# Kernel tuning notes

Hardware: AMD Instinct MI355X
Metric: run time of the kernel (lower is better)

The kernel has to match this reference:

```python
import jax, jax.numpy as jnp
import numpy as np

D_MODEL = 1024
N_HEADS = 16
D_K = D_MODEL // N_HEADS


def setup_inputs() -> dict:
    key = jax.random.key(0)
    ks = jax.random.split(key, 7)
    B, S = 2, 2048
    q = jax.random.normal(ks[0], (B, S, D_MODEL), dtype=jnp.float32)
    k = jax.random.normal(ks[1], (B, S, D_MODEL), dtype=jnp.float32)
    v = jax.random.normal(ks[2], (B, S, D_MODEL), dtype=jnp.float32)
    mask = jnp.ones((B, 1, S, S), dtype=bool)
    scale = 1.0 / np.sqrt(D_MODEL)
    w_q = jax.random.normal(ks[3], (D_MODEL, D_MODEL), dtype=jnp.float32) * scale
    w_k = jax.random.normal(ks[4], (D_MODEL, D_MODEL), dtype=jnp.float32) * scale
    w_v = jax.random.normal(ks[5], (D_MODEL, D_MODEL), dtype=jnp.float32) * scale
    w_o = jax.random.normal(ks[6], (D_MODEL, D_MODEL), dtype=jnp.float32) * scale
    return {"q": q, "k": k, "v": v, "mask": mask,
            "w_q": w_q, "w_k": w_k, "w_v": w_v, "w_o": w_o}


def reference(q, k, v, mask, w_q, w_k, w_v, w_o):
    B, S, _ = q.shape
    # projections (nn.Linear: x @ W^T, no bias)
    def split_heads(x):  # [B,S,D] -> [B,H,S,d_k]
        return x.reshape(B, -1, N_HEADS, D_K).transpose(0, 2, 1, 3)
    query = split_heads(q @ w_q.T)
    key_h = split_heads(k @ w_k.T)
    value = split_heads(v @ w_v.T)
    # naive scaled dot-product attention: full [B,H,S,S] scores materialized
    scores = jnp.einsum('bhqd,bhkd->bhqk', query, key_h) / jnp.sqrt(
        jnp.asarray(D_K, query.dtype))
    scores = jnp.where(mask, scores, jnp.asarray(-1e9, scores.dtype))
    attn = jax.nn.softmax(scores, axis=-1)  # dropout p=0.0 -> identity
    x = jnp.einsum('bhqk,bhkd->bhqd', attn, value)
    x = x.transpose(0, 2, 1, 3).reshape(B, S, N_HEADS * D_K)
    return x @ w_o.T
```

## Files before the change

### kernel.cpp

```cpp
#include <hip/hip_runtime.h>
#include <hip/hip_bf16.h>
#include <math.h>

typedef __bf16 bf16;
typedef __bf16 bf16x8 __attribute__((ext_vector_type(8)));
typedef float f32x4 __attribute__((ext_vector_type(4)));
typedef float f32x16 __attribute__((ext_vector_type(16)));
typedef unsigned u32x4 __attribute__((ext_vector_type(4)));

#define MFMA16(a, b, c) __builtin_amdgcn_mfma_f32_16x16x32_bf16((a), (b), (c), 0, 0, 0)
#define MFMA32(a, b, c) __builtin_amdgcn_mfma_f32_32x32x16_bf16((a), (b), (c), 0, 0, 0)

__device__ __forceinline__ void gl_lds16(const void* g, void* l) {
    __builtin_amdgcn_global_load_lds(
        (__attribute__((address_space(1))) void*)(g),
        (__attribute__((address_space(3))) void*)(l),
        16, 0, 0);
}

__device__ __forceinline__ unsigned cvt_pk_bf16(float lo, float hi) {
    unsigned r;
    asm("v_cvt_pk_bf16_f32 %0, %1, %2" : "=v"(r) : "v"(lo), "v"(hi));
    return r;
}

__global__ __launch_bounds__(256) void cvt7(
    const float* __restrict__ w0, const float* __restrict__ w1,
    const float* __restrict__ w2, const float* __restrict__ w3,
    const float* __restrict__ x0, const float* __restrict__ x1,
    const float* __restrict__ x2, bf16* __restrict__ dst) {
    const int z = blockIdx.y;
    const float* src;
    bf16* out;
    if (z < 4) {
        if (blockIdx.x >= 512) return;
        src = (z == 0) ? w0 : (z == 1) ? w1 : (z == 2) ? w2 : w3;
        out = dst + (size_t)z * 1048576;
    } else {
        src = (z == 4) ? x0 : (z == 5) ? x1 : x2;
        out = dst + 4 * 1048576 + (size_t)(z - 4) * 4194304;
    }
    const int i = (blockIdx.x * 256 + threadIdx.x) * 8;
    float4 a = ((const float4*)(src + i))[0];
    float4 b = ((const float4*)(src + i))[1];
    bf16x8 o;
    o[0] = (bf16)a.x; o[1] = (bf16)a.y; o[2] = (bf16)a.z; o[3] = (bf16)a.w;
    o[4] = (bf16)b.x; o[5] = (bf16)b.y; o[6] = (bf16)b.z; o[7] = (bf16)b.w;
    *(bf16x8*)(out + i) = o;
}

template <int EP>
__device__ __forceinline__ void gemm_bf(const bf16* __restrict__ A,
                                        const bf16* __restrict__ B,
                                        void* __restrict__ Cv,
                                        const int m0, const int n0,
                                        bf16* __restrict__ As,
                                        bf16* __restrict__ Bs) {
    constexpr int K = 1024;

    const int t = threadIdx.x;
    const int lane = t & 63;
    const int w = t >> 6;
    const int wm = (w >> 2) * 64;
    const int wn = (w & 3) * 32;
    const int lr = lane & 15;
    const int lq8 = (lane >> 4) * 8;
    const int rq = (lane >> 4) * 4;

    f32x4 acc[4][2] = {};

    const int srow = t >> 2;
    const int sch = (t & 3) * 8;
    char* lA = (char*)As;
    char* lB = (char*)Bs;

#define QSTAGE(buf, k0)                                                              \
    do {                                                                             \
        gl_lds16(A + (size_t)(m0 + srow) * K + (k0) + sch,                           \
                 lA + (buf) * 8192 + t * 16);                                        \
        gl_lds16(B + (size_t)(n0 + srow) * K + (k0) + sch,                           \
                 lB + (buf) * 8192 + t * 16);                                        \
    } while (0)

    QSTAGE(0, 0);
    __syncthreads();

    int cur = 0;
    for (int k0 = 0; k0 < K; k0 += 32) {
        if (k0 + 32 < K) QSTAGE(cur ^ 1, k0 + 32);

        bf16x8 af[4], bfr[2];
#pragma unroll
        for (int i = 0; i < 4; ++i)
            af[i]  = *(const bf16x8*)&As[cur * 4096 + (wm + i * 16 + lr) * 32 + lq8];
#pragma unroll
        for (int i = 0; i < 2; ++i)
            bfr[i] = *(const bf16x8*)&Bs[cur * 4096 + (wn + i * 16 + lr) * 32 + lq8];
#pragma unroll
        for (int mi = 0; mi < 4; ++mi)
#pragma unroll
            for (int ni = 0; ni < 2; ++ni)
                acc[mi][ni] = MFMA16(af[mi], bfr[ni], acc[mi][ni]);

        __syncthreads();
        cur ^= 1;
    }
#undef QSTAGE

#pragma unroll
    for (int mi = 0; mi < 4; ++mi) {
#pragma unroll
        for (int ni = 0; ni < 2; ++ni) {
#pragma unroll
            for (int r = 0; r < 4; ++r) {
                const int m = m0 + wm + mi * 16 + rq + r;
                const int n = n0 + wn + ni * 16 + lr;
                const float vv = acc[mi][ni][r];
                if constexpr (EP == 0) {
                    bf16* C = (bf16*)Cv;
                    const int b = m >> 11, s = m & 2047;
                    const int h = n >> 6,  d = n & 63;
                    C[(((size_t)(b * 16 + h)) * 2048 + s) * 64 + d] = (bf16)vv;
                } else if constexpr (EP == 1) {
                    float* C = (float*)Cv;
                    C[(size_t)m * 1024 + n] = vv;
                } else {
                    bf16* C = (bf16*)Cv;
                    C[((size_t)(n >> 11) * 1024 + m) * 2048 + (n & 2047)] = (bf16)vv;
                }
            }
        }
    }
}

__global__ __launch_bounds__(512, 6) void qkv_bf(
    const bf16* __restrict__ Xq, const bf16* __restrict__ Xk,
    const bf16* __restrict__ Xv, const bf16* __restrict__ Wc,
    bf16* __restrict__ Qb, bf16* __restrict__ Kb, bf16* __restrict__ Vb) {
    __shared__ __align__(16) bf16 As[2 * 128 * 32];
    __shared__ __align__(16) bf16 Bs[2 * 128 * 32];
    const int z = blockIdx.z;
    if (z == 0)
        gemm_bf<0>(Xq, Wc, Qb, blockIdx.x * 128, blockIdx.y * 128, As, Bs);
    else if (z == 1)
        gemm_bf<0>(Xk, Wc + 1048576, Kb, blockIdx.x * 128, blockIdx.y * 128, As, Bs);
    else
        gemm_bf<2>(Wc + 2 * 1048576, Xv, Vb, blockIdx.y * 128, blockIdx.x * 128, As, Bs);
}

__global__ __launch_bounds__(512, 4) void out_gemm(
    const bf16* __restrict__ X, const bf16* __restrict__ W, float* __restrict__ C) {
    constexpr int K = 1024;
    __shared__ __align__(16) bf16 As[2][128 * 32];
    __shared__ __align__(16) bf16 Bs[2][64 * 32];

    const int t = threadIdx.x;
    const int lane = t & 63;
    const int w = t >> 6;
    const int wm = (w >> 1) * 32;
    const int wn = (w & 1) * 32;
    const int lr = lane & 15;
    const int lq8 = (lane >> 4) * 8;
    const int rq = (lane >> 4) * 4;
    const int m0 = blockIdx.x * 128, n0 = blockIdx.y * 64;

    f32x4 acc[2][2] = {};

    const int srow = t >> 2;
    const int sch = (t & 3) * 8;
    char* lA = (char*)As;
    char* lB = (char*)Bs;

#define OSTAGE(buf, k0)                                                              \
    do {                                                                             \
        gl_lds16(X + (size_t)(m0 + srow) * K + (k0) + sch,                           \
                 lA + (buf) * 8192 + t * 16);                                        \
        if (t < 256)                                                                 \
            gl_lds16(W + (size_t)(n0 + srow) * K + (k0) + sch,                       \
                     lB + (buf) * 4096 + t * 16);                                    \
    } while (0)

    OSTAGE(0, 0);
    __syncthreads();

    int cur = 0;
    for (int k0 = 0; k0 < K; k0 += 32) {
        if (k0 + 32 < K) OSTAGE(cur ^ 1, k0 + 32);

        bf16x8 af[2], bfr[2];
#pragma unroll
        for (int i = 0; i < 2; ++i) {
            af[i]  = *(const bf16x8*)&As[cur][(wm + i * 16 + lr) * 32 + lq8];
            bfr[i] = *(const bf16x8*)&Bs[cur][(wn + i * 16 + lr) * 32 + lq8];
        }
#pragma unroll
        for (int mi = 0; mi < 2; ++mi)
#pragma unroll
            for (int ni = 0; ni < 2; ++ni)
                acc[mi][ni] = MFMA16(af[mi], bfr[ni], acc[mi][ni]);

        __syncthreads();
        cur ^= 1;
    }
#undef OSTAGE

#pragma unroll
    for (int mi = 0; mi < 2; ++mi)
#pragma unroll
        for (int ni = 0; ni < 2; ++ni)
#pragma unroll
            for (int r = 0; r < 4; ++r) {
                const int m = m0 + wm + mi * 16 + rq + r;
                const int n = n0 + wn + ni * 16 + lr;
                C[(size_t)m * 1024 + n] = acc[mi][ni][r];
            }
}

template <int MODE>
__device__ __forceinline__ void gemm_f32tok(const void* __restrict__ Av,
                                            const void* __restrict__ Bv,
                                            bf16* __restrict__ C,
                                            const int m0, const int n0,
                                            bf16* __restrict__ As,
                                            bf16* __restrict__ Bs) {
    constexpr int K = 1024;

    const int t = threadIdx.x;
    const int lane = t & 63;
    const int w = t >> 6;
    const int wm = (w & 1) * 64;
    const int wn = (w >> 1) * 64;
    const int lr = lane & 15;
    const int lq8 = (lane >> 4) * 8;
    const int rq = (lane >> 4) * 4;

    f32x4 acc[4][4] = {};
    const int srow = t >> 2;
    const int sch = (t & 3) * 8;
    const int ar = t >> 1;
    const int ac = (t & 1) * 16;
    char* lA = (char*)As;
    char* lB = (char*)Bs;

    for (int k0 = 0; k0 < K; k0 += 32) {
        if constexpr (MODE == 0) {
            const float* X = (const float*)Av;
            const float* p = X + (size_t)(m0 + ar) * K + k0 + ac;
            float4 f0 = ((const float4*)p)[0], f1 = ((const float4*)p)[1];
            float4 f2 = ((const float4*)p)[2], f3 = ((const float4*)p)[3];
            bf16x8 o0, o1;
            o0[0]=(bf16)f0.x; o0[1]=(bf16)f0.y; o0[2]=(bf16)f0.z; o0[3]=(bf16)f0.w;
            o0[4]=(bf16)f1.x; o0[5]=(bf16)f1.y; o0[6]=(bf16)f1.z; o0[7]=(bf16)f1.w;
            o1[0]=(bf16)f2.x; o1[1]=(bf16)f2.y; o1[2]=(bf16)f2.z; o1[3]=(bf16)f2.w;
            o1[4]=(bf16)f3.x; o1[5]=(bf16)f3.y; o1[6]=(bf16)f3.z; o1[7]=(bf16)f3.w;
            *(bf16x8*)&As[ar * 32 + ac]     = o0;
            *(bf16x8*)&As[ar * 32 + ac + 8] = o1;
        } else {
            const bf16* X = (const bf16*)Av;
            gl_lds16(X + (size_t)(m0 + srow) * K + k0 + sch,      lA + t * 16);
            gl_lds16(X + (size_t)(m0 + 64 + srow) * K + k0 + sch, lA + 4096 + t * 16);
        }
        if constexpr (MODE == 2) {
            const float* X = (const float*)Bv;
            const float* p = X + (size_t)(n0 + ar) * K + k0 + ac;
            float4 f0 = ((const float4*)p)[0], f1 = ((const float4*)p)[1];
            float4 f2 = ((const float4*)p)[2], f3 = ((const float4*)p)[3];
            bf16x8 o0, o1;
            o0[0]=(bf16)f0.x; o0[1]=(bf16)f0.y; o0[2]=(bf16)f0.z; o0[3]=(bf16)f0.w;
            o0[4]=(bf16)f1.x; o0[5]=(bf16)f1.y; o0[6]=(bf16)f1.z; o0[7]=(bf16)f1.w;
            o1[0]=(bf16)f2.x; o1[1]=(bf16)f2.y; o1[2]=(bf16)f2.z; o1[3]=(bf16)f2.w;
            o1[4]=(bf16)f3.x; o1[5]=(bf16)f3.y; o1[6]=(bf16)f3.z; o1[7]=(bf16)f3.w;
            *(bf16x8*)&Bs[ar * 32 + ac]     = o0;
            *(bf16x8*)&Bs[ar * 32 + ac + 8] = o1;
        } else {
            const bf16* W = (const bf16*)Bv;
            gl_lds16(W + (size_t)(n0 + srow) * K + k0 + sch,      lB + t * 16);
            gl_lds16(W + (size_t)(n0 + 64 + srow) * K + k0 + sch, lB + 4096 + t * 16);
        }
        __syncthreads();

        bf16x8 af[4], bfr[4];
#pragma unroll
        for (int i = 0; i < 4; ++i) {
            af[i]  = *(const bf16x8*)&As[(wm + i * 16 + lr) * 32 + lq8];
            bfr[i] = *(const bf16x8*)&Bs[(wn + i * 16 + lr) * 32 + lq8];
        }
#pragma unroll
        for (int mi = 0; mi < 4; ++mi)
#pragma unroll
            for (int ni = 0; ni < 4; ++ni)
                acc[mi][ni] = MFMA16(af[mi], bfr[ni], acc[mi][ni]);
        __syncthreads();
    }

#pragma unroll
    for (int mi = 0; mi < 4; ++mi) {
#pragma unroll
        for (int ni = 0; ni < 4; ++ni) {
#pragma unroll
            for (int r = 0; r < 4; ++r) {
                const int m = m0 + wm + mi * 16 + rq + r;
                const int n = n0 + wn + ni * 16 + lr;
                const float vv = acc[mi][ni][r];
                if constexpr (MODE == 0) {
                    const int b = m >> 11, s = m & 2047;
                    const int h = n >> 6,  d = n & 63;
                    C[(((size_t)(b * 16 + h)) * 2048 + s) * 64 + d] = (bf16)vv;
                } else {
                    C[((size_t)(n >> 11) * 1024 + m) * 2048 + (n & 2047)] = (bf16)vv;
                }
            }
        }
    }
}

__global__ __launch_bounds__(256, 2) void qkv_f32(
    const float* __restrict__ q, const float* __restrict__ k, const float* __restrict__ v,
    const bf16* __restrict__ Wc, bf16* __restrict__ Qb, bf16* __restrict__ Kb,
    bf16* __restrict__ Vb) {
    __shared__ __align__(16) bf16 As[128 * 32];
    __shared__ __align__(16) bf16 Bs[128 * 32];
    const int z = blockIdx.z;
    if (z == 0)
        gemm_f32tok<0>(q, Wc, Qb, blockIdx.x * 128, blockIdx.y * 128, As, Bs);
    else if (z == 1)
        gemm_f32tok<0>(k, Wc + 1048576, Kb, blockIdx.x * 128, blockIdx.y * 128, As, Bs);
    else
        gemm_f32tok<2>(Wc + 2 * 1048576, v, Vb, blockIdx.y * 128, blockIdx.x * 128, As, Bs);
}

__global__ __launch_bounds__(512, 4) void attn_kernel(
    const bf16* __restrict__ Qb, const bf16* __restrict__ Kb,
    const bf16* __restrict__ Vb, bf16* __restrict__ Xb) {
    constexpr int S = 2048;

    __shared__ __align__(16) bf16 smem[17408];

    const int t = threadIdx.x;
    const int lane = t & 63;
    const int w = t >> 6;
    const int wg = w & 3;
    const int kh = w >> 2;
    const int l31 = lane & 31;
    const int half = lane >> 5;

    const int lin = blockIdx.x;
    const int g = lin >> 3;
    const int bh = (lin & 7) + 8 * (g & 3);
    const int q0 = (g >> 2) * 128 + wg * 32;

    const bf16* Q  = Qb + (size_t)bh * S * 64;
    const bf16* Kh = Kb + (size_t)bh * S * 64;
    const bf16* Vh = Vb + (size_t)bh * 64 * S;

    const float qscale = 0.125f * 1.4426950408889634f;
    bf16x8 qf[4];
#pragma unroll
    for (int c = 0; c < 4; ++c) {
        bf16x8 v0 = *(const bf16x8*)(Q + (size_t)(q0 + l31) * 64 + c * 16 + half * 8);
#pragma unroll
        for (int e = 0; e < 8; ++e) v0[e] = (bf16)((float)v0[e] * qscale);
        qf[c] = v0;
    }

    f32x16 od[2] = {};
    float ls0 = 0.f, ls1 = 0.f, ls2 = 0.f, ls3 = 0.f;

    const int tt = t & 255;
    const int sr = tt >> 2;
    const int sc = (tt & 3) * 2;
    const bf16* pKg = Kh + ((size_t)kh * 1024 + sr) * 64 + sc * 8;
    const bf16* pVg = Vh + (size_t)sr * S + kh * 1024 + sc * 8;
    bf16* KsH = smem + kh * 4096;
    bf16* VsH = smem + 8192 + kh * 4096;
    int wKo[2];
#pragma unroll
    for (int c = 0; c < 2; ++c)
        wKo[c] = (sr >> 1) * 128 + ((((sr & 1) << 3) + sc + c) ^ ((sr >> 1) & 15)) * 8;

    bf16x8 pk[2], pv[2];
#pragma unroll
    for (int c = 0; c < 2; ++c) {
        pk[c] = *(const bf16x8*)(pKg + c * 8);
        pv[c] = *(const bf16x8*)(pVg + c * 8);
    }

    const int fbase = (l31 >> 1) * 128;
    const int fb8 = (l31 & 1) << 3;
    const int fsw = l31 >> 1;

    for (int j = 0; j < 16; ++j) {
        __syncthreads();
#pragma unroll
        for (int c = 0; c < 2; ++c) {
            *(bf16x8*)&KsH[wKo[c]] = pk[c];
            *(bf16x8*)&VsH[wKo[c]] = pv[c];
        }
        __syncthreads();

        f32x16 sacc[2] = {};
#pragma unroll
        for (int kt = 0; kt < 2; ++kt) {
#pragma unroll
            for (int c = 0; c < 4; ++c) {
                bf16x8 kf = *(const bf16x8*)
                    &KsH[kt * 2048 + fbase + ((fb8 + c * 2 + half) ^ fsw) * 8];
                sacc[kt] = MFMA32(kf, qf[c], sacc[kt]);
            }
        }

        if (j + 1 < 16) {
            pKg += 4096;
            pVg += 64;
#pragma unroll
            for (int c = 0; c < 2; ++c) {
                pk[c] = *(const bf16x8*)(pKg + c * 8);
                pv[c] = *(const bf16x8*)(pVg + c * 8);
            }
        }

#pragma unroll
        for (int kt = 0; kt < 2; ++kt) {
            float ex[16];
#pragma unroll
            for (int r = 0; r < 16; ++r)
                ex[r] = exp2f(sacc[kt][r]);
            ls0 += ex[0] + ex[4] + ex[8]  + ex[12];
            ls1 += ex[1] + ex[5] + ex[9]  + ex[13];
            ls2 += ex[2] + ex[6] + ex[10] + ex[14];
            ls3 += ex[3] + ex[7] + ex[11] + ex[15];

            unsigned pa[8];
#pragma unroll
            for (int c2 = 0; c2 < 2; ++c2) {
#pragma unroll
                for (int wd = 0; wd < 2; ++wd) {
                    unsigned x = cvt_pk_bf16(ex[c2 * 8 + wd * 2 + 0], ex[c2 * 8 + wd * 2 + 1]);
                    unsigned y = cvt_pk_bf16(ex[c2 * 8 + wd * 2 + 4], ex[c2 * 8 + wd * 2 + 5]);
                    asm("v_permlane32_swap_b32 %0, %1" : "+v"(x), "+v"(y));
                    pa[c2 * 4 + wd]     = x;
                    pa[c2 * 4 + wd + 2] = y;
                }
            }

#pragma unroll
            for (int c2 = 0; c2 < 2; ++c2) {
                u32x4 aw;
                aw[0] = pa[c2 * 4 + 0]; aw[1] = pa[c2 * 4 + 1];
                aw[2] = pa[c2 * 4 + 2]; aw[3] = pa[c2 * 4 + 3];
                bf16x8 ap = __builtin_bit_cast(bf16x8, aw);
#pragma unroll
                for (int dt = 0; dt < 2; ++dt) {
                    const int cgv = kt * 4 + c2 * 2 + half;
                    bf16x8 vf = *(const bf16x8*)
                        &VsH[dt * 2048 + fbase + ((fb8 + cgv) ^ fsw) * 8];
                    od[dt] = MFMA32(ap, vf, od[dt]);
                }
            }
        }
    }

    float lsum = ls0 + ls1 + ls2 + ls3;
    float ltot = lsum + __shfl_xor(lsum, 32);

    __syncthreads();
    float* fsm = (float*)smem;
    const int so = (wg * 64 + lane) * 34;
    if (kh == 1) {
        fsm[so + 32] = ltot;
#pragma unroll
        for (int r = 0; r < 16; ++r) {
            fsm[so + r]      = od[0][r];
            fsm[so + 16 + r] = od[1][r];
        }
    }
    __syncthreads();
    if (kh == 0) {
        ltot += fsm[so + 32];
        const float inv = 1.f / fmaxf(ltot, 1e-30f);
        const int b = bh >> 4, hh = bh & 15;
#pragma unroll
        for (int r = 0; r < 16; ++r) {
            const int qrow = (r & 3) + 8 * (r >> 2) + 4 * half;
            const float invr = __shfl(inv, qrow);
            const size_t base = ((size_t)(b * 2048 + q0 + qrow)) * 1024 + hh * 64;
            Xb[base + l31]      = (bf16)((od[0][r] + fsm[so + r]) * invr);
            Xb[base + 32 + l31] = (bf16)((od[1][r] + fsm[so + 16 + r]) * invr);
        }
    }
}

extern "C" void kernel_launch(void* const* d_in, const int* in_sizes, int n_in,
                              void* d_out, int out_size, void* d_ws, size_t ws_size,
                              hipStream_t stream) {
    const float* q  = (const float*)d_in[0];
    const float* k  = (const float*)d_in[1];
    const float* v  = (const float*)d_in[2];
    const float* wq = (const float*)d_in[4];
    const float* wk = (const float*)d_in[5];
    const float* wv = (const float*)d_in[6];
    const float* wo = (const float*)d_in[7];
    float* out = (float*)d_out;

    const bool big = ws_size >= (size_t)64 * 1024 * 1024;
    bf16* Wc = (bf16*)d_ws;
    const dim3 blk(256);

    if (big) {
        bf16* Xq = Wc + 4 * 1048576;
        bf16* Xk = Xq + 4194304;
        bf16* Xv = Xk + 4194304;
        bf16* Qb = Xv + 4194304;
        bf16* Kb = Qb + 4194304;
        bf16* Vb = Kb + 4194304;
        bf16* Xb = Vb + 4194304;
        cvt7<<<dim3(2048, 7), blk, 0, stream>>>(wq, wk, wv, wo, q, k, v, Wc);
        qkv_bf<<<dim3(32, 8, 3), dim3(512), 0, stream>>>(Xq, Xk, Xv, Wc, Qb, Kb, Vb);
        attn_kernel<<<dim3(512), dim3(512), 0, stream>>>(Qb, Kb, Vb, Xb);
        out_gemm<<<dim3(32, 16), dim3(512), 0, stream>>>(Xb, Wc + 3 * 1048576, out);
    } else {
        bf16* Qb = Wc + 4 * 1048576;
        bf16* Kb = Qb + 4194304;
        bf16* Vb = Kb + 4194304;
        bf16* Xb = Vb + 4194304;
        cvt7<<<dim3(512, 4), blk, 0, stream>>>(wq, wk, wv, wo, q, k, v, Wc);
        qkv_f32<<<dim3(32, 8, 3), blk, 0, stream>>>(q, k, v, Wc, Qb, Kb, Vb);
        attn_kernel<<<dim3(512), dim3(512), 0, stream>>>(Qb, Kb, Vb, Xb);
        out_gemm<<<dim3(32, 16), dim3(512), 0, stream>>>(Xb, Wc + 3 * 1048576, out);
    }
}
```

Before: 236.9 us.

## Fuse fp32-to-bf16 activation conversion into QKV projection GEMM staging

The QKV GEMM now reads the fp32 q/k/v activations directly. It loads them into registers during the prefetch stage and converts them to bf16 when writing LDS after the MFMA work. The separate conversion pass for activations is dropped, and cvt7 now converts only the weights. This removes a full write and read of three 4M-element bf16 activation buffers. In exchange, each fp32 tile is re-read once for every N-tile block, which doubles the global bytes on the activation side. Staging also goes through registers instead of direct global-to-LDS loads, which adds register pressure and VALU conversion work inside the main loop.

```diff
diff --git a/kernel.cpp b/kernel.cpp
--- a/kernel.cpp
+++ b/kernel.cpp
@@ -49,9 +49,9 @@
     *(bf16x8*)(out + i) = o;
 }
 
-template <int EP>
-__device__ __forceinline__ void gemm_bf(const bf16* __restrict__ A,
-                                        const bf16* __restrict__ B,
+template <int EP, int AF32, int BF32>
+__device__ __forceinline__ void gemm_bf(const void* __restrict__ Av,
+                                        const void* __restrict__ Bv,
                                         void* __restrict__ Cv,
                                         const int m0, const int n0,
                                         bf16* __restrict__ As,
@@ -74,20 +74,60 @@
     char* lA = (char*)As;
     char* lB = (char*)Bs;
 
-#define QSTAGE(buf, k0)                                                              \
-    do {                                                                             \
-        gl_lds16(A + (size_t)(m0 + srow) * K + (k0) + sch,                           \
-                 lA + (buf) * 8192 + t * 16);                                        \
-        gl_lds16(B + (size_t)(n0 + srow) * K + (k0) + sch,                           \
-                 lB + (buf) * 8192 + t * 16);                                        \
-    } while (0)
-
-    QSTAGE(0, 0);
+    const bf16* Ab = (const bf16*)Av;
+    const bf16* Bb = (const bf16*)Bv;
+    const float* Af = (const float*)Av;
+    const float* Bf = (const float*)Bv;
+
+    float4 fa0, fa1, fb0, fb1;
+
+#define LOAD_F32A(k0)                                                                \
+    do {                                                                             \
+        const float* P = Af + (size_t)(m0 + srow) * K + (k0) + sch;                  \
+        fa0 = ((const float4*)P)[0]; fa1 = ((const float4*)P)[1];                    \
+    } while (0)
+#define WRITE_F32A(buf)                                                              \
+    do {                                                                             \
+        bf16x8 o;                                                                    \
+        o[0]=(bf16)fa0.x; o[1]=(bf16)fa0.y; o[2]=(bf16)fa0.z; o[3]=(bf16)fa0.w;      \
+        o[4]=(bf16)fa1.x; o[5]=(bf16)fa1.y; o[6]=(bf16)fa1.z; o[7]=(bf16)fa1.w;      \
+        *(bf16x8*)&As[(buf) * 4096 + srow * 32 + sch] = o;                           \
+    } while (0)
+#define LOAD_F32B(k0)                                                                \
+    do {                                                                             \
+        const float* P = Bf + (size_t)(n0 + srow) * K + (k0) + sch;                  \
+        fb0 = ((const float4*)P)[0]; fb1 = ((const float4*)P)[1];                    \
+    } while (0)
+#define WRITE_F32B(buf)                                                              \
+    do {                                                                             \
+        bf16x8 o;                                                                    \
+        o[0]=(bf16)fb0.x; o[1]=(bf16)fb0.y; o[2]=(bf16)fb0.z; o[3]=(bf16)fb0.w;      \
+        o[4]=(bf16)fb1.x; o[5]=(bf16)fb1.y; o[6]=(bf16)fb1.z; o[7]=(bf16)fb1.w;      \
+        *(bf16x8*)&Bs[(buf) * 4096 + srow * 32 + sch] = o;                           \
+    } while (0)
+#define STAGE_ISSUE(buf, k0)                                                         \
+    do {                                                                             \
+        if constexpr (AF32) LOAD_F32A(k0);                                           \
+        else gl_lds16(Ab + (size_t)(m0 + srow) * K + (k0) + sch,                     \
+                      lA + (buf) * 8192 + t * 16);                                   \
+        if constexpr (BF32) LOAD_F32B(k0);                                           \
+        else gl_lds16(Bb + (size_t)(n0 + srow) * K + (k0) + sch,                     \
+                      lB + (buf) * 8192 + t * 16);                                   \
+    } while (0)
+#define STAGE_WRITE(buf)                                                             \
+    do {                                                                             \
+        if constexpr (AF32) WRITE_F32A(buf);                                         \
+        if constexpr (BF32) WRITE_F32B(buf);                                         \
+    } while (0)
+
+    STAGE_ISSUE(0, 0);
+    STAGE_WRITE(0);
     __syncthreads();
 
     int cur = 0;
     for (int k0 = 0; k0 < K; k0 += 32) {
-        if (k0 + 32 < K) QSTAGE(cur ^ 1, k0 + 32);
+        const bool nxt = (k0 + 32 < K);
+        if (nxt) STAGE_ISSUE(cur ^ 1, k0 + 32);
 
         bf16x8 af[4], bfr[2];
 #pragma unroll
@@ -102,10 +142,17 @@
             for (int ni = 0; ni < 2; ++ni)
                 acc[mi][ni] = MFMA16(af[mi], bfr[ni], acc[mi][ni]);
 
+        if (nxt) STAGE_WRITE(cur ^ 1);
+
         __syncthreads();
         cur ^= 1;
     }
-#undef QSTAGE
+#undef STAGE_WRITE
+#undef STAGE_ISSUE
+#undef WRITE_F32B
+#undef LOAD_F32B
+#undef WRITE_F32A
+#undef LOAD_F32A
 
 #pragma unroll
     for (int mi = 0; mi < 4; ++mi) {
@@ -134,18 +181,18 @@
 }
 
 __global__ __launch_bounds__(512, 6) void qkv_bf(
-    const bf16* __restrict__ Xq, const bf16* __restrict__ Xk,
-    const bf16* __restrict__ Xv, const bf16* __restrict__ Wc,
+    const float* __restrict__ q, const float* __restrict__ k,
+    const float* __restrict__ v, const bf16* __restrict__ Wc,
     bf16* __restrict__ Qb, bf16* __restrict__ Kb, bf16* __restrict__ Vb) {
     __shared__ __align__(16) bf16 As[2 * 128 * 32];
     __shared__ __align__(16) bf16 Bs[2 * 128 * 32];
     const int z = blockIdx.z;
     if (z == 0)
-        gemm_bf<0>(Xq, Wc, Qb, blockIdx.x * 128, blockIdx.y * 128, As, Bs);
+        gemm_bf<0, 1, 0>(q, Wc, Qb, blockIdx.x * 128, blockIdx.y * 128, As, Bs);
     else if (z == 1)
-        gemm_bf<0>(Xk, Wc + 1048576, Kb, blockIdx.x * 128, blockIdx.y * 128, As, Bs);
+        gemm_bf<0, 1, 0>(k, Wc + 1048576, Kb, blockIdx.x * 128, blockIdx.y * 128, As, Bs);
     else
-        gemm_bf<2>(Wc + 2 * 1048576, Xv, Vb, blockIdx.y * 128, blockIdx.x * 128, As, Bs);
+        gemm_bf<2, 0, 1>(Wc + 2 * 1048576, v, Vb, blockIdx.y * 128, blockIdx.x * 128, As, Bs);
 }
 
 __global__ __launch_bounds__(512, 4) void out_gemm(
@@ -507,15 +554,12 @@
     const dim3 blk(256);
 
     if (big) {
-        bf16* Xq = Wc + 4 * 1048576;
-        bf16* Xk = Xq + 4194304;
-        bf16* Xv = Xk + 4194304;
-        bf16* Qb = Xv + 4194304;
+        bf16* Qb = Wc + 4 * 1048576 + 3 * 4194304;
         bf16* Kb = Qb + 4194304;
         bf16* Vb = Kb + 4194304;
         bf16* Xb = Vb + 4194304;
-        cvt7<<<dim3(2048, 7), blk, 0, stream>>>(wq, wk, wv, wo, q, k, v, Wc);
-        qkv_bf<<<dim3(32, 8, 3), dim3(512), 0, stream>>>(Xq, Xk, Xv, Wc, Qb, Kb, Vb);
+        cvt7<<<dim3(512, 4), blk, 0, stream>>>(wq, wk, wv, wo, q, k, v, Wc);
+        qkv_bf<<<dim3(32, 8, 3), dim3(512), 0, stream>>>(q, k, v, Wc, Qb, Kb, Vb);
         attn_kernel<<<dim3(512), dim3(512), 0, stream>>>(Qb, Kb, Vb, Xb);
         out_gemm<<<dim3(32, 16), dim3(512), 0, stream>>>(Xb, Wc + 3 * 1048576, out);
     } else {
```

New measurement: 252.1 us. 6.4% more time.
